# Kernel optimization log

Hardware: AMD Instinct MI355X
Metric: run time of the kernel (lower is better)

Reference implementation:

```python
import jax, jax.numpy as jnp
import numpy as np

P, G, UV = 5, 40000, 256          # n_parts, gs_num (visible UV texels), uv_size
ZD, FD, HD = 32, 64, 32           # latent_z_dim, latent_f_dim, latent_h_dim
H1, L1 = 128, 3                   # mlp1 hidden dim, fc layers
H2, L2 = 128, 3                   # mlp2 hidden dim, fc layers
CC, LC = 64, 4                    # cnn hidden channels, cnn hidden layers


def _mlp_params(key, din, hid, nlayers, dout, nparts):
    ks = jax.random.split(key, 3)
    s = lambda f: 1.0 / np.sqrt(f)
    return dict(
        w_in=jax.random.normal(ks[0], (nparts, din, hid), jnp.float32) * s(din),
        b_in=jnp.zeros((nparts, hid), jnp.float32),
        w_hid=jax.random.normal(ks[1], (nparts, nlayers - 1, hid, hid), jnp.float32) * s(hid),
        b_hid=jnp.zeros((nparts, nlayers - 1, hid), jnp.float32),
        w_out=jax.random.normal(ks[2], (nparts, hid, dout), jnp.float32) * s(hid),
        b_out=jnp.zeros((nparts, dout), jnp.float32),
    )


def setup_inputs() -> dict:
    key = jax.random.key(0)
    ks = jax.random.split(key, 12)
    d1 = FD + ZD
    d2 = d1 + 3 + 11
    inp = {
        'latent_z': jax.random.normal(ks[2], (G, ZD), jnp.float32),
        'latent_f': jax.random.normal(ks[3], (P, FD), jnp.float32),
        'cano_xyz': jax.random.normal(ks[4], (G, 3), jnp.float32),
    }
    for k, v in _mlp_params(ks[0], d1, H1, L1, 11, P).items():
        inp['mlp1_' + k] = v
    for k, v in _mlp_params(ks[1], d2, H2, L2, HD, P).items():
        inp['mlp2_' + k] = v
    inp['conv_in_w'] = jax.random.normal(ks[5], (CC, HD, 3, 3), jnp.float32) * (1.0 / np.sqrt(HD * 9))
    inp['conv_in_b'] = jnp.zeros((CC,), jnp.float32)
    inp['conv_hid_w'] = jax.random.normal(ks[6], (LC - 1, CC, CC, 3, 3), jnp.float32) * (1.0 / np.sqrt(CC * 9))
    inp['conv_hid_b'] = jnp.zeros((LC - 1, CC), jnp.float32)
    inp['conv_out_w'] = jax.random.normal(ks[7], (3, CC, 3, 3), jnp.float32) * (1.0 / np.sqrt(CC * 9))
    inp['conv_out_b'] = jnp.zeros((3,), jnp.float32)
    inp['gs_part'] = jax.random.randint(ks[8], (G,), 0, P, jnp.int32)
    inp['uv_idx'] = jax.random.permutation(ks[9], UV * UV)[:G].astype(jnp.int32)  # unique visible texels
    return inp


def _part_mlp(x, w_in, b_in, w_hid, b_hid, w_out, b_out, part):
    # x: [G, D]; weights stacked over parts. Run every part's MLP, gather by part id.
    h = jax.nn.leaky_relu(jnp.einsum('gd,pdh->pgh', x, w_in) + b_in[:, None, :])
    for l in range(w_hid.shape[1]):
        h = jax.nn.leaky_relu(jnp.einsum('pgh,pho->pgo', h, w_hid[:, l]) + b_hid[:, l][:, None, :])
    out = jnp.einsum('pgh,pho->pgo', h, w_out) + b_out[:, None, :]  # [P, G, O]
    return out[part, jnp.arange(out.shape[1])]                       # [G, O]


def _conv(x, w, b):
    y = jax.lax.conv_general_dilated(x, w, (1, 1), 'SAME',
                                     dimension_numbers=('NCHW', 'OIHW', 'NCHW'))
    return y + b[None, :, None, None]


def _instance_norm(x, eps=1e-5):
    m = x.mean(axis=(2, 3), keepdims=True)
    v = x.var(axis=(2, 3), keepdims=True)
    return (x - m) / jnp.sqrt(v + eps)


def reference(latent_z, latent_f, cano_xyz,
              mlp1_w_in, mlp1_b_in, mlp1_w_hid, mlp1_b_hid, mlp1_w_out, mlp1_b_out,
              mlp2_w_in, mlp2_b_in, mlp2_w_hid, mlp2_b_hid, mlp2_w_out, mlp2_b_out,
              conv_in_w, conv_in_b, conv_hid_w, conv_hid_b, conv_out_w, conv_out_b,
              gs_part, uv_idx):
    feat_f = latent_f[gs_part]                                  # [G, FD] per-part feature gather
    x1 = jnp.concatenate([feat_f, latent_z], axis=-1)           # [G, FD+ZD]
    attrs = _part_mlp(x1, mlp1_w_in, mlp1_b_in, mlp1_w_hid, mlp1_b_hid,
                      mlp1_w_out, mlp1_b_out, gs_part)          # [G, 11] gaussian attrs
    x2 = jnp.concatenate([x1, cano_xyz, attrs], axis=-1)        # [G, FD+ZD+3+11]
    h = _part_mlp(x2, mlp2_w_in, mlp2_b_in, mlp2_w_hid, mlp2_b_hid,
                  mlp2_w_out, mlp2_b_out, gs_part)              # [G, HD]
    # scatter per-gaussian features back into the UV map (uvmask-indexed texels)
    uvmap = jnp.zeros((UV * UV, h.shape[-1]), h.dtype).at[uv_idx].add(h)
    x = uvmap.T.reshape(1, h.shape[-1], UV, UV)                 # [1, HD, UV, UV]
    # CNN refinement: conv -> (relu, conv, instance_norm) x (LC-1) -> conv -> sigmoid
    x = _conv(x, conv_in_w, conv_in_b)
    for l in range(conv_hid_w.shape[0]):
        x = _instance_norm(_conv(jax.nn.relu(x), conv_hid_w[l], conv_hid_b[l]))
    x = _conv(x, conv_out_w, conv_out_b)
    return jax.nn.sigmoid(x)                                    # [1, 3, UV, UV]
```

## Files before the change

### kernel.cpp

```cpp
#include <hip/hip_runtime.h>

#define G_N 40000
#define P_N 5
#define PIX 65536
#define XP 136
#define SP 40

typedef short short8 __attribute__((ext_vector_type(8)));
typedef short short4v __attribute__((ext_vector_type(4)));
typedef float f32x4 __attribute__((ext_vector_type(4)));
#define MFMA16(a, b, c) __builtin_amdgcn_mfma_f32_16x16x32_bf16(a, b, c, 0, 0, 0)

__device__ __forceinline__ short f2b(float f) {
    unsigned u = __builtin_bit_cast(unsigned, f);
    unsigned r = (u + 0x7fffu + ((u >> 16) & 1u)) >> 16;
    return (short)r;
}
__device__ __forceinline__ float b2f(short s) {
    unsigned u = ((unsigned)(unsigned short)s) << 16;
    return __builtin_bit_cast(float, u);
}


__global__ __launch_bounds__(256) void hist_k(const int* __restrict__ part,
                                              int* __restrict__ counts, int n) {
    __shared__ int s_c[P_N];
    if (threadIdx.x < P_N) s_c[threadIdx.x] = 0;
    __syncthreads();
    int g = blockIdx.x * 256 + threadIdx.x;
    if (g < n) atomicAdd(&s_c[part[g]], 1);
    __syncthreads();
    if (threadIdx.x < P_N) atomicAdd(&counts[threadIdx.x], s_c[threadIdx.x]);
}

__global__ void offs_k(const int* __restrict__ counts, int* __restrict__ offs) {
    if (threadIdx.x == 0) {
        int o = 0;
        for (int p = 0; p < P_N; ++p) {
            offs[p] = o;
            o += (counts[p] + 63) & ~63;
        }
        offs[P_N] = o;
    }
}

__global__ __launch_bounds__(256) void scatter_k(const int* __restrict__ part,
                                                 const int* __restrict__ offs,
                                                 int* __restrict__ cursors,
                                                 int* __restrict__ perm, int n) {
    const int t = threadIdx.x;
    const int g = blockIdx.x * 256 + t;
    const int p = (g < n) ? part[g] : -1;
    const int lane = t & 63;
    const int wid = t >> 6;
    __shared__ int s_wc[4][P_N];
    __shared__ int s_base[P_N];
    const unsigned long long lmask = (1ull << lane) - 1ull;
    int myrank = 0;
    for (int pp = 0; pp < P_N; ++pp) {
        unsigned long long m = __ballot(p == pp);
        if (p == pp) myrank = __popcll(m & lmask);
        if (lane == 0) s_wc[wid][pp] = __popcll(m);
    }
    __syncthreads();
    if (t < P_N) {
        int tot = s_wc[0][t] + s_wc[1][t] + s_wc[2][t] + s_wc[3][t];
        s_base[t] = atomicAdd(&cursors[t], tot);
    }
    __syncthreads();
    if (g < n) {
        int pre = 0;
        #pragma unroll
        for (int w2 = 0; w2 < 4; ++w2) if (w2 < wid) pre += s_wc[w2][p];
        perm[offs[p] + s_base[p] + pre + myrank] = g;
    }
}


__device__ __forceinline__ float mseg(int l, const float* __restrict__ src,
                                      int DIN, int DOUT, int NP, int pps) {
    const int pn = NP * 128;
    const int p = l / pn;
    const int r = l - p * pn;
    const int n = r >> 7, k = r & 127;
    return (n < DOUT && k < DIN) ? src[p * pps + k * DOUT + n] : 0.f;
}
__device__ __forceinline__ float cseg(int l, const float* __restrict__ src, int CIN) {
    const int per = 9 * 64 * CIN;
    const int ll = l / per;
    int rem = l - ll * per;
    const int tap = rem / (64 * CIN);
    rem -= tap * 64 * CIN;
    const int och = rem / CIN;
    const int ci = rem - och * CIN;
    return src[((ll * 64 + och) * CIN + ci) * 9 + tap];
}

__global__ __launch_bounds__(256) void prep_k(
        const float* __restrict__ m1wi, const float* __restrict__ m1wh,
        const float* __restrict__ m1wo, const float* __restrict__ m2wi,
        const float* __restrict__ m2wh, const float* __restrict__ m2wo,
        const float* __restrict__ cinw, const float* __restrict__ chw,
        short* __restrict__ wb) {
    const int idx = blockIdx.x * 256 + threadIdx.x;
    if (idx >= 651264) return;
    float v;
    if      (idx < 81920)  v = mseg(idx,          m1wi,         96, 128, 128, 12288);
    else if (idx < 163840) v = mseg(idx - 81920,  m1wh,        128, 128, 128, 32768);
    else if (idx < 245760) v = mseg(idx - 163840, m1wh + 16384,128, 128, 128, 32768);
    else if (idx < 256000) v = mseg(idx - 245760, m1wo,        128,  11,  16, 1408);
    else if (idx < 337920) v = mseg(idx - 256000, m2wi,        110, 128, 128, 14080);
    else if (idx < 419840) v = mseg(idx - 337920, m2wh,        128, 128, 128, 32768);
    else if (idx < 501760) v = mseg(idx - 419840, m2wh + 16384,128, 128, 128, 32768);
    else if (idx < 522240) v = mseg(idx - 501760, m2wo,        128,  32,  32, 4096);
    else if (idx < 540672) v = cseg(idx - 522240, cinw, 32);
    else                   v = cseg(idx - 540672, chw, 64);
    wb[idx] = f2b(v);
}


template<int NKC, bool ACT>
__device__ __forceinline__ void wcompute(const short8 (&A)[4][NKC],
                                         const short* __restrict__ wt,
                                         const float* __restrict__ bias,
                                         short* dst) {
    const int ln = threadIdx.x & 15, lq = threadIdx.x >> 4;
    short8 Bc[2][NKC];
    float bsc[2];
    #pragma unroll
    for (int j = 0; j < 2; ++j) {
        #pragma unroll
        for (int kc = 0; kc < NKC; ++kc)
            Bc[j][kc] = *(const short8*)(wt + (j * 16 + ln) * 128 + kc * 32 + lq * 8);
        bsc[j] = bias[j * 16 + ln];
    }
    #pragma unroll
    for (int g = 0; g < 4; ++g) {
        short8 Bn[2][NKC];
        float bsn[2];
        if (g < 3) {
            #pragma unroll
            for (int j = 0; j < 2; ++j) {
                #pragma unroll
                for (int kc = 0; kc < NKC; ++kc)
                    Bn[j][kc] = *(const short8*)(wt + ((g * 2 + 2 + j) * 16 + ln) * 128 + kc * 32 + lq * 8);
                bsn[j] = bias[(g * 2 + 2 + j) * 16 + ln];
            }
        }
        f32x4 acc[4][2];
        #pragma unroll
        for (int mt = 0; mt < 4; ++mt)
            #pragma unroll
            for (int j = 0; j < 2; ++j) {
                f32x4 a = {bsc[j], bsc[j], bsc[j], bsc[j]};
                acc[mt][j] = a;
            }
        #pragma unroll
        for (int kc = 0; kc < NKC; ++kc)
            #pragma unroll
            for (int mt = 0; mt < 4; ++mt)
                #pragma unroll
                for (int j = 0; j < 2; ++j)
                    acc[mt][j] = MFMA16(A[mt][kc], Bc[j][kc], acc[mt][j]);
        #pragma unroll
        for (int mt = 0; mt < 4; ++mt)
            #pragma unroll
            for (int j = 0; j < 2; ++j)
                #pragma unroll
                for (int r = 0; r < 4; ++r) {
                    float v = acc[mt][j][r];
                    if (ACT) v = fmaxf(v, 0.01f * v);
                    dst[(mt * 16 + lq * 4 + r) * XP + (g * 2 + j) * 16 + ln] = f2b(v);
                }
        if (g < 3) {
            #pragma unroll
            for (int j = 0; j < 2; ++j) {
                #pragma unroll
                for (int kc = 0; kc < NKC; ++kc) Bc[j][kc] = Bn[j][kc];
                bsc[j] = bsn[j];
            }
        }
    }
}

__device__ __forceinline__ void preload4(short8 (&A)[4][4], const short* s) {
    const int ln = threadIdx.x & 15, lq = threadIdx.x >> 4;
    #pragma unroll
    for (int mt = 0; mt < 4; ++mt)
        #pragma unroll
        for (int kc = 0; kc < 4; ++kc)
            A[mt][kc] = *(const short8*)(s + (mt * 16 + ln) * XP + kc * 32 + lq * 8);
}

__global__ __launch_bounds__(64, 2) void mlp_k(
        const float* __restrict__ latent_z, const float* __restrict__ latent_f,
        const float* __restrict__ cano,
        const short* __restrict__ wt1i, const float* __restrict__ b1i,
        const short* __restrict__ wt1h0, const short* __restrict__ wt1h1,
        const float* __restrict__ b1h,
        const short* __restrict__ wt1o, const float* __restrict__ b1o,
        const short* __restrict__ wt2i, const float* __restrict__ b2i,
        const short* __restrict__ wt2h0, const short* __restrict__ wt2h1,
        const float* __restrict__ b2h,
        const short* __restrict__ wt2o, const float* __restrict__ b2o,
        const int* __restrict__ uv_idx, const int* __restrict__ perm,
        const int* __restrict__ offs, const int* __restrict__ counts,
        unsigned short* __restrict__ uvmap ) {
    __shared__ short s_h[64 * XP];
    __shared__ short s_c4[64 * SP];
    __shared__ int s_g[64];
    __shared__ int s_uv[64];

    const int t = threadIdx.x;
    const int ln = t & 15, lq = t >> 4;
    const int pos0 = blockIdx.x * 64;
    if (pos0 >= offs[P_N]) return;
    int p = 0;
    #pragma unroll
    for (int q = 1; q < P_N; ++q) if (pos0 >= offs[q]) p = q;
    const int vend = offs[p] + counts[p];

    {
        const int pos = pos0 + t;
        const int g = (pos < vend) ? perm[pos] : -1;
        s_g[t] = g;
        s_uv[t] = (g >= 0) ? uv_idx[g] : 0;
    }
    for (int i = t; i < 64 * SP / 2; i += 64) ((int*)s_c4)[i] = 0;
    __syncthreads();

    for (int i = t; i < 64 * 16; i += 64) {
        const int g = i >> 4, k4 = (i & 15) * 4;
        const float4 v = *(const float4*)(latent_f + p * 64 + k4);
        short4v o = {f2b(v.x), f2b(v.y), f2b(v.z), f2b(v.w)};
        *(short4v*)(s_h + g * XP + k4) = o;
    }
    for (int i = t; i < 64 * 8; i += 64) {
        const int g = i >> 3, k4 = (i & 7) * 4;
        const int gg = s_g[g];
        short4v o = {0, 0, 0, 0};
        if (gg >= 0) {
            const float4 v = *(const float4*)(latent_z + gg * 32 + k4);
            o[0] = f2b(v.x); o[1] = f2b(v.y); o[2] = f2b(v.z); o[3] = f2b(v.w);
        }
        *(short4v*)(s_h + g * XP + 64 + k4) = o;
    }
    for (int i = t; i < 64 * 3; i += 64) {
        const int g = i / 3, k = i - g * 3;
        const int gg = s_g[g];
        s_c4[g * SP + k] = (gg >= 0) ? f2b(cano[gg * 3 + k]) : 0;
    }
    __syncthreads();

    short8 A1[4][3];
    #pragma unroll
    for (int mt = 0; mt < 4; ++mt)
        #pragma unroll
        for (int kc = 0; kc < 3; ++kc)
            A1[mt][kc] = *(const short8*)(s_h + (mt * 16 + ln) * XP + kc * 32 + lq * 8);
    __syncthreads();

    wcompute<3, true>(A1, wt1i + p * 16384, b1i + p * 128, s_h);
    __syncthreads();
    {
        short8 Ah[4][4];
        preload4(Ah, s_h); __syncthreads();
        wcompute<4, true>(Ah, wt1h0 + p * 16384, b1h + (p * 2 + 0) * 128, s_h);
        __syncthreads();
        preload4(Ah, s_h); __syncthreads();
        wcompute<4, true>(Ah, wt1h1 + p * 16384, b1h + (p * 2 + 1) * 128, s_h);
        __syncthreads();
        preload4(Ah, s_h); __syncthreads();
        short8 B[4];
        #pragma unroll
        for (int kc = 0; kc < 4; ++kc)
            B[kc] = *(const short8*)(wt1o + p * 2048 + ln * 128 + kc * 32 + lq * 8);
        const float bs = (ln < 11) ? b1o[p * 11 + ln] : 0.f;
        #pragma unroll
        for (int mt = 0; mt < 4; ++mt) {
            f32x4 acc = {bs, bs, bs, bs};
            #pragma unroll
            for (int kc = 0; kc < 4; ++kc) acc = MFMA16(Ah[mt][kc], B[kc], acc);
            if (ln < 11) {
                #pragma unroll
                for (int r = 0; r < 4; ++r)
                    s_c4[(mt * 16 + lq * 4 + r) * SP + 3 + ln] = f2b(acc[r]);
            }
        }
    }
    __syncthreads();

    {
        short8 A2[4][4];
        #pragma unroll
        for (int mt = 0; mt < 4; ++mt) {
            A2[mt][0] = A1[mt][0]; A2[mt][1] = A1[mt][1]; A2[mt][2] = A1[mt][2];
            A2[mt][3] = *(const short8*)(s_c4 + (mt * 16 + ln) * SP + lq * 8);
        }
        __syncthreads();
        wcompute<4, true>(A2, wt2i + p * 16384, b2i + p * 128, s_h);
    }
    __syncthreads();
    {
        short8 Ah[4][4];
        preload4(Ah, s_h); __syncthreads();
        wcompute<4, true>(Ah, wt2h0 + p * 16384, b2h + (p * 2 + 0) * 128, s_h);
        __syncthreads();
        preload4(Ah, s_h); __syncthreads();
        wcompute<4, true>(Ah, wt2h1 + p * 16384, b2h + (p * 2 + 1) * 128, s_h);
        __syncthreads();
        preload4(Ah, s_h);
        #pragma unroll
        for (int nt = 0; nt < 2; ++nt) {
            short8 B[4];
            #pragma unroll
            for (int kc = 0; kc < 4; ++kc)
                B[kc] = *(const short8*)(wt2o + p * 4096 + (nt * 16 + ln) * 128 + kc * 32 + lq * 8);
            const float bs = b2o[p * 32 + nt * 16 + ln];
            #pragma unroll
            for (int mt = 0; mt < 4; ++mt) {
                f32x4 acc = {bs, bs, bs, bs};
                #pragma unroll
                for (int kc = 0; kc < 4; ++kc) acc = MFMA16(Ah[mt][kc], B[kc], acc);
                #pragma unroll
                for (int r = 0; r < 4; ++r) {
                    const int m = mt * 16 + lq * 4 + r;
                    const int g = s_g[m];
                    if (g >= 0)
                        uvmap[s_uv[m] * 32 + nt * 16 + ln] = (unsigned short)f2b(acc[r]);
                }
            }
        }
    }
}


template<int CIN, int TRANS, bool STATS>
__global__ __launch_bounds__(128, 2) void conv_k(
        const unsigned short* __restrict__ in,
        const short* __restrict__ wt,
        const float* __restrict__ bias,
        const float* __restrict__ psum, const float* __restrict__ psq,
        unsigned short* __restrict__ out,
        float* __restrict__ ssum, float* __restrict__ ssq) {
    constexpr int CS = CIN + 8;
    constexpr int NKC = CIN / 32;
    constexpr int RUNS = CIN / 8;
    __shared__ short s_in[10 * 18 * CS];
    __shared__ float s_mr[2][64];
    __shared__ float s_red[2][2][64];

    const int t = threadIdx.x;
    const int ln = t & 15, lq = (t >> 4) & 3;
    const int w2 = t >> 6;
    const int tx0 = blockIdx.x * 16, ty0 = blockIdx.y * 8;

    if (TRANS == 2 && t < 64) {
        const float m = psum[t] * (1.f / PIX);
        const float vv = psq[t] * (1.f / PIX) - m * m;
        s_mr[0][t] = m;
        s_mr[1][t] = rsqrtf(vv + 1e-5f);
    }
    if (TRANS == 2) __syncthreads();

    short8 Bc[NKC][4];
    #pragma unroll
    for (int kc = 0; kc < NKC; ++kc)
        #pragma unroll
        for (int nt = 0; nt < 4; ++nt)
            Bc[kc][nt] = *(const short8*)(wt + (nt * 16 + ln) * CIN + kc * 32 + lq * 8);

    for (int i = t; i < 180 * RUNS; i += 128) {
        const int sp = i / RUNS, run = i - sp * RUNS;
        const int r = sp / 18, c = sp - r * 18;
        const int gy = ty0 + r - 1, gx = tx0 + c - 1;
        short* dst = &s_in[(r * 18 + c) * CS + run * 8];
        if (gy >= 0 && gy < 256 && gx >= 0 && gx < 256) {
            short8 v = *(const short8*)(in + ((gy * 256 + gx) * CIN + run * 8));
            if (TRANS == 0) {
                *(short8*)dst = v;
            } else {
                short8 o;
                #pragma unroll
                for (int j = 0; j < 8; ++j) {
                    float f = b2f(v[j]);
                    if (TRANS == 2) f = (f - s_mr[0][run * 8 + j]) * s_mr[1][run * 8 + j];
                    o[j] = f2b(fmaxf(f, 0.f));
                }
                *(short8*)dst = o;
            }
        } else {
            short8 z = {0, 0, 0, 0, 0, 0, 0, 0};
            *(short8*)dst = z;
        }
    }
    __syncthreads();

    f32x4 acc[4][4];
    {
        float bs[4];
        #pragma unroll
        for (int nt = 0; nt < 4; ++nt) bs[nt] = bias[nt * 16 + ln];
        #pragma unroll
        for (int mt = 0; mt < 4; ++mt)
            #pragma unroll
            for (int nt = 0; nt < 4; ++nt) {
                f32x4 a = {bs[nt], bs[nt], bs[nt], bs[nt]};
                acc[mt][nt] = a;
            }
    }

    #pragma unroll
    for (int tap = 0; tap < 9; ++tap) {
        short8 Bn[NKC][4];
        if (tap < 8) {
            const short* wnext = wt + (tap + 1) * 64 * CIN;
            #pragma unroll
            for (int kc = 0; kc < NKC; ++kc)
                #pragma unroll
                for (int nt = 0; nt < 4; ++nt)
                    Bn[kc][nt] = *(const short8*)(wnext + (nt * 16 + ln) * CIN + kc * 32 + lq * 8);
        }
        const int dy = tap / 3, dx = tap - dy * 3;
        #pragma unroll
        for (int kc = 0; kc < NKC; ++kc) {
            short8 A[4];
            #pragma unroll
            for (int mt = 0; mt < 4; ++mt)
                A[mt] = *(const short8*)&s_in[((w2 * 4 + mt + dy) * 18 + ln + dx) * CS + kc * 32 + lq * 8];
            #pragma unroll
            for (int mt = 0; mt < 4; ++mt)
                #pragma unroll
                for (int nt = 0; nt < 4; ++nt)
                    acc[mt][nt] = MFMA16(A[mt], Bc[kc][nt], acc[mt][nt]);
        }
        if (tap < 8) {
            #pragma unroll
            for (int kc = 0; kc < NKC; ++kc)
                #pragma unroll
                for (int nt = 0; nt < 4; ++nt)
                    Bc[kc][nt] = Bn[kc][nt];
        }
    }

    #pragma unroll
    for (int nt = 0; nt < 4; ++nt) {
        float ls = 0.f, lsq = 0.f;
        #pragma unroll
        for (int mt = 0; mt < 4; ++mt) {
            const int gy = ty0 + w2 * 4 + mt;
            #pragma unroll
            for (int r = 0; r < 4; ++r) {
                const float v = acc[mt][nt][r];
                const int gx = tx0 + lq * 4 + r;
                out[(gy * 256 + gx) * 64 + nt * 16 + ln] = (unsigned short)f2b(v);
                if (STATS) { ls += v; lsq = fmaf(v, v, lsq); }
            }
        }
        if (STATS) {
            ls  += __shfl_xor(ls, 16, 64);
            ls  += __shfl_xor(ls, 32, 64);
            lsq += __shfl_xor(lsq, 16, 64);
            lsq += __shfl_xor(lsq, 32, 64);
            if (lq == 0 && (t & 32) == 0) {
                s_red[w2][0][nt * 16 + ln] = ls;
                s_red[w2][1][nt * 16 + ln] = lsq;
            }
        }
    }
    if (STATS) {
        __syncthreads();
        if (t < 64) {
            atomicAdd(&ssum[t], s_red[0][0][t] + s_red[1][0][t]);
            atomicAdd(&ssq[t],  s_red[0][1][t] + s_red[1][1][t]);
        }
    }
}

__global__ __launch_bounds__(128) void convout_k(
        const unsigned short* __restrict__ in,
        const float* __restrict__ w,
        const float* __restrict__ bias,
        const float* __restrict__ psum, const float* __restrict__ psq,
        float* __restrict__ out) {
    constexpr int CS = 72;
    __shared__ short s_in[10 * 18 * CS];
    __shared__ float s_w[3][9][64];
    __shared__ float s_mr[2][64];

    const int t = threadIdx.x;
    const int tx0 = blockIdx.x * 16, ty0 = blockIdx.y * 8;
    if (t < 64) {
        const float m = psum[t] * (1.f / PIX);
        const float vv = psq[t] * (1.f / PIX) - m * m;
        s_mr[0][t] = m;
        s_mr[1][t] = rsqrtf(vv + 1e-5f);
    }
    __syncthreads();

    for (int i = t; i < 180 * 8; i += 128) {
        const int sp = i >> 3, run = i & 7;
        const int r = sp / 18, c = sp - r * 18;
        const int gy = ty0 + r - 1, gx = tx0 + c - 1;
        short* dst = &s_in[(r * 18 + c) * CS + run * 8];
        if (gy >= 0 && gy < 256 && gx >= 0 && gx < 256) {
            short8 v = *(const short8*)(in + ((gy * 256 + gx) * 64 + run * 8));
            short8 o;
            #pragma unroll
            for (int j = 0; j < 8; ++j) {
                const float f = (b2f(v[j]) - s_mr[0][run * 8 + j]) * s_mr[1][run * 8 + j];
                o[j] = f2b(f);
            }
            *(short8*)dst = o;
        } else {
            short8 z = {0, 0, 0, 0, 0, 0, 0, 0};
            *(short8*)dst = z;
        }
    }
    for (int i = t; i < 1728; i += 128) {
        const int o = i / 576;
        const int rem = i - o * 576;
        const int tap = rem >> 6;
        const int ci = rem & 63;
        s_w[o][tap][ci] = w[o * 576 + ci * 9 + tap];
    }
    __syncthreads();

    const int py = t >> 4, px = t & 15;
    float a0 = bias[0], a1 = bias[1], a2 = bias[2];
    for (int tap = 0; tap < 9; ++tap) {
        const int dy = tap / 3, dx = tap % 3;
        const short* rp = &s_in[((py + dy) * 18 + (px + dx)) * CS];
        #pragma unroll
        for (int c8 = 0; c8 < 8; ++c8) {
            short8 v = *(const short8*)(rp + c8 * 8);
            #pragma unroll
            for (int j = 0; j < 8; ++j) {
                const float f = b2f(v[j]);
                const int ci = c8 * 8 + j;
                a0 = fmaf(f, s_w[0][tap][ci], a0);
                a1 = fmaf(f, s_w[1][tap][ci], a1);
                a2 = fmaf(f, s_w[2][tap][ci], a2);
            }
        }
    }
    const int pix = (ty0 + py) * 256 + tx0 + px;
    out[pix]           = 1.f / (1.f + expf(-a0));
    out[PIX + pix]     = 1.f / (1.f + expf(-a1));
    out[2 * PIX + pix] = 1.f / (1.f + expf(-a2));
}


extern "C" void kernel_launch(void* const* d_in, const int* in_sizes, int n_in,
                              void* d_out, int out_size, void* d_ws, size_t ws_size,
                              hipStream_t stream) {
    (void)in_sizes; (void)n_in; (void)out_size; (void)ws_size;
    const float* latent_z = (const float*)d_in[0];
    const float* latent_f = (const float*)d_in[1];
    const float* cano     = (const float*)d_in[2];
    const float* m1wi = (const float*)d_in[3];
    const float* m1bi = (const float*)d_in[4];
    const float* m1wh = (const float*)d_in[5];
    const float* m1bh = (const float*)d_in[6];
    const float* m1wo = (const float*)d_in[7];
    const float* m1bo = (const float*)d_in[8];
    const float* m2wi = (const float*)d_in[9];
    const float* m2bi = (const float*)d_in[10];
    const float* m2wh = (const float*)d_in[11];
    const float* m2bh = (const float*)d_in[12];
    const float* m2wo = (const float*)d_in[13];
    const float* m2bo = (const float*)d_in[14];
    const float* cinw = (const float*)d_in[15];
    const float* cinb = (const float*)d_in[16];
    const float* chw  = (const float*)d_in[17];
    const float* chb  = (const float*)d_in[18];
    const float* cow  = (const float*)d_in[19];
    const float* cob  = (const float*)d_in[20];
    const int* gs_part = (const int*)d_in[21];
    const int* uv_idx  = (const int*)d_in[22];

    float* ws = (float*)d_ws;
    unsigned short* actA = (unsigned short*)ws;
    unsigned short* actB = (unsigned short*)(ws + 2097152);
    unsigned short* uvmap = actB;

    short* wb = (short*)(ws + 4194304);
    short* wt1i  = wb;
    short* wt1h0 = wb + 81920;
    short* wt1h1 = wb + 163840;
    short* wt1o  = wb + 245760;
    short* wt2i  = wb + 256000;
    short* wt2h0 = wb + 337920;
    short* wt2h1 = wb + 419840;
    short* wt2o  = wb + 501760;
    short* cwt_in  = wb + 522240;
    short* cwt_hid = wb + 540672;

    float* small = ws + 4194304 + 330000;
    int* counts  = (int*)small;
    int* cursors = counts + 8;
    int* offs    = cursors + 8;
    float* ssum  = small + 32;
    float* ssq   = ssum + 192;
    int* perm    = (int*)(ssq + 192);

    hipMemsetAsync(uvmap, 0, (size_t)PIX * 32 * sizeof(unsigned short), stream);
    hipMemsetAsync(small, 0, 1024 * sizeof(float), stream);

    hist_k<<<157, 256, 0, stream>>>(gs_part, counts, G_N);
    offs_k<<<1, 64, 0, stream>>>(counts, offs);
    scatter_k<<<157, 256, 0, stream>>>(gs_part, offs, cursors, perm, G_N);

    prep_k<<<2544, 256, 0, stream>>>(m1wi, m1wh, m1wo, m2wi, m2wh, m2wo, cinw, chw, wb);

    mlp_k<<<630, 64, 0, stream>>>(latent_z, latent_f, cano,
        wt1i, m1bi, wt1h0, wt1h1, m1bh, wt1o, m1bo,
        wt2i, m2bi, wt2h0, wt2h1, m2bh, wt2o, m2bo,
        uv_idx, perm, offs, counts, uvmap);

    dim3 cgrid(16, 32);
    conv_k<32, 0, false><<<cgrid, 128, 0, stream>>>(uvmap, cwt_in, cinb,
        nullptr, nullptr, actA, nullptr, nullptr);
    conv_k<64, 1, true><<<cgrid, 128, 0, stream>>>(actA, cwt_hid, chb,
        nullptr, nullptr, actB, ssum, ssq);
    conv_k<64, 2, true><<<cgrid, 128, 0, stream>>>(actB, cwt_hid + 36864, chb + 64,
        ssum, ssq, actA, ssum + 64, ssq + 64);
    conv_k<64, 2, true><<<cgrid, 128, 0, stream>>>(actA, cwt_hid + 73728, chb + 128,
        ssum + 64, ssq + 64, actB, ssum + 128, ssq + 128);
    convout_k<<<cgrid, 128, 0, stream>>>(actB, cow, cob,
        ssum + 128, ssq + 128, (float*)d_out);
}
```

Measured before the change: 269.1 us.

## Split MLP layers across two waves with ping-pong LDS and transposed MFMA

The MLP kernel now runs 128 threads per block, with each wave computing half of the output columns of every layer. Activations ping-pong between two LDS buffers, which removes the extra barrier the old in-place update needed between reading and writing. The MFMA operands are swapped so each lane holds four consecutive output channels, allowing vectorized bf16 stores to LDS, to the uvmap and in the conv kernels. Conv statistics are now reduced with shuffles and atomics directly instead of through a shared buffer. The costs are more LDS per block, duplicated A-operand loads in both waves, and more global atomics.

```diff
diff --git a/kernel.cpp b/kernel.cpp
--- a/kernel.cpp
+++ b/kernel.cpp
@@ -4,7 +4,7 @@
 #define P_N 5
 #define PIX 65536
 #define XP 136
-#define SP 40
+#define SP 32
 
 typedef short short8 __attribute__((ext_vector_type(8)));
 typedef short short4v __attribute__((ext_vector_type(4)));
@@ -120,71 +120,51 @@
 
 
 template<int NKC, bool ACT>
-__device__ __forceinline__ void wcompute(const short8 (&A)[4][NKC],
-                                         const short* __restrict__ wt,
-                                         const float* __restrict__ bias,
-                                         short* dst) {
-    const int ln = threadIdx.x & 15, lq = threadIdx.x >> 4;
-    short8 Bc[2][NKC];
-    float bsc[2];
+__device__ __forceinline__ void wlayer(const short8 (&A)[4][NKC],
+                                       const short* __restrict__ wt,
+                                       const float* __restrict__ bias,
+                                       short* dst, int ln, int lq, int w) {
     #pragma unroll
-    for (int j = 0; j < 2; ++j) {
+    for (int g = 0; g < 2; ++g) {
+        short8 W[2][NKC];
+        f32x4 b4[2];
+        #pragma unroll
+        for (int j = 0; j < 2; ++j) {
+            const int ntg = w * 4 + g * 2 + j;
+            #pragma unroll
+            for (int kc = 0; kc < NKC; ++kc)
+                W[j][kc] = *(const short8*)(wt + (ntg * 16 + ln) * 128 + kc * 32 + lq * 8);
+            b4[j] = *(const f32x4*)(bias + ntg * 16 + lq * 4);
+        }
+        f32x4 acc[4][2];
+        #pragma unroll
+        for (int mt = 0; mt < 4; ++mt)
+            #pragma unroll
+            for (int j = 0; j < 2; ++j) acc[mt][j] = b4[j];
         #pragma unroll
         for (int kc = 0; kc < NKC; ++kc)
-            Bc[j][kc] = *(const short8*)(wt + (j * 16 + ln) * 128 + kc * 32 + lq * 8);
-        bsc[j] = bias[j * 16 + ln];
-    }
-    #pragma unroll
-    for (int g = 0; g < 4; ++g) {
-        short8 Bn[2][NKC];
-        float bsn[2];
-        if (g < 3) {
+            #pragma unroll
+            for (int mt = 0; mt < 4; ++mt)
+                #pragma unroll
+                for (int j = 0; j < 2; ++j)
+                    acc[mt][j] = MFMA16(W[j][kc], A[mt][kc], acc[mt][j]);
+        #pragma unroll
+        for (int mt = 0; mt < 4; ++mt)
             #pragma unroll
             for (int j = 0; j < 2; ++j) {
-                #pragma unroll
-                for (int kc = 0; kc < NKC; ++kc)
-                    Bn[j][kc] = *(const short8*)(wt + ((g * 2 + 2 + j) * 16 + ln) * 128 + kc * 32 + lq * 8);
-                bsn[j] = bias[(g * 2 + 2 + j) * 16 + ln];
+                const int ntg = w * 4 + g * 2 + j;
+                f32x4 a = acc[mt][j];
+                if (ACT) {
+                    #pragma unroll
+                    for (int r = 0; r < 4; ++r) a[r] = fmaxf(a[r], 0.01f * a[r]);
+                }
+                short4v o = {f2b(a[0]), f2b(a[1]), f2b(a[2]), f2b(a[3])};
+                *(short4v*)(dst + (mt * 16 + ln) * XP + ntg * 16 + lq * 4) = o;
             }
-        }
-        f32x4 acc[4][2];
-        #pragma unroll
-        for (int mt = 0; mt < 4; ++mt)
-            #pragma unroll
-            for (int j = 0; j < 2; ++j) {
-                f32x4 a = {bsc[j], bsc[j], bsc[j], bsc[j]};
-                acc[mt][j] = a;
-            }
-        #pragma unroll
-        for (int kc = 0; kc < NKC; ++kc)
-            #pragma unroll
-            for (int mt = 0; mt < 4; ++mt)
-                #pragma unroll
-                for (int j = 0; j < 2; ++j)
-                    acc[mt][j] = MFMA16(A[mt][kc], Bc[j][kc], acc[mt][j]);
-        #pragma unroll
-        for (int mt = 0; mt < 4; ++mt)
-            #pragma unroll
-            for (int j = 0; j < 2; ++j)
-                #pragma unroll
-                for (int r = 0; r < 4; ++r) {
-                    float v = acc[mt][j][r];
-                    if (ACT) v = fmaxf(v, 0.01f * v);
-                    dst[(mt * 16 + lq * 4 + r) * XP + (g * 2 + j) * 16 + ln] = f2b(v);
-                }
-        if (g < 3) {
-            #pragma unroll
-            for (int j = 0; j < 2; ++j) {
-                #pragma unroll
-                for (int kc = 0; kc < NKC; ++kc) Bc[j][kc] = Bn[j][kc];
-                bsc[j] = bsn[j];
-            }
-        }
-    }
-}
-
-__device__ __forceinline__ void preload4(short8 (&A)[4][4], const short* s) {
-    const int ln = threadIdx.x & 15, lq = threadIdx.x >> 4;
+    }
+}
+
+__device__ __forceinline__ void preload4(short8 (&A)[4][4], const short* s, int ln, int lq) {
     #pragma unroll
     for (int mt = 0; mt < 4; ++mt)
         #pragma unroll
@@ -192,7 +172,7 @@
             A[mt][kc] = *(const short8*)(s + (mt * 16 + ln) * XP + kc * 32 + lq * 8);
 }
 
-__global__ __launch_bounds__(64, 2) void mlp_k(
+__global__ __launch_bounds__(128, 2) void mlp_k(
         const float* __restrict__ latent_z, const float* __restrict__ latent_f,
         const float* __restrict__ cano,
         const short* __restrict__ wt1i, const float* __restrict__ b1i,
@@ -206,13 +186,15 @@
         const int* __restrict__ uv_idx, const int* __restrict__ perm,
         const int* __restrict__ offs, const int* __restrict__ counts,
         unsigned short* __restrict__ uvmap ) {
-    __shared__ short s_h[64 * XP];
+    __shared__ short s_a[64 * XP];
+    __shared__ short s_b[64 * XP];
     __shared__ short s_c4[64 * SP];
     __shared__ int s_g[64];
     __shared__ int s_uv[64];
 
     const int t = threadIdx.x;
-    const int ln = t & 15, lq = t >> 4;
+    const int ln = t & 15, lq = (t >> 4) & 3;
+    const int w = t >> 6;
     const int pos0 = blockIdx.x * 64;
     if (pos0 >= offs[P_N]) return;
     int p = 0;
@@ -220,22 +202,22 @@
     for (int q = 1; q < P_N; ++q) if (pos0 >= offs[q]) p = q;
     const int vend = offs[p] + counts[p];
 
-    {
+    if (t < 64) {
         const int pos = pos0 + t;
         const int g = (pos < vend) ? perm[pos] : -1;
         s_g[t] = g;
         s_uv[t] = (g >= 0) ? uv_idx[g] : 0;
     }
-    for (int i = t; i < 64 * SP / 2; i += 64) ((int*)s_c4)[i] = 0;
-    __syncthreads();
-
-    for (int i = t; i < 64 * 16; i += 64) {
+    for (int i = t; i < 64 * SP / 2; i += 128) ((int*)s_c4)[i] = 0;
+    __syncthreads();
+
+    for (int i = t; i < 64 * 16; i += 128) {
         const int g = i >> 4, k4 = (i & 15) * 4;
         const float4 v = *(const float4*)(latent_f + p * 64 + k4);
         short4v o = {f2b(v.x), f2b(v.y), f2b(v.z), f2b(v.w)};
-        *(short4v*)(s_h + g * XP + k4) = o;
-    }
-    for (int i = t; i < 64 * 8; i += 64) {
+        *(short4v*)(s_a + g * XP + k4) = o;
+    }
+    for (int i = t; i < 64 * 8; i += 128) {
         const int g = i >> 3, k4 = (i & 7) * 4;
         const int gg = s_g[g];
         short4v o = {0, 0, 0, 0};
@@ -243,9 +225,9 @@
             const float4 v = *(const float4*)(latent_z + gg * 32 + k4);
             o[0] = f2b(v.x); o[1] = f2b(v.y); o[2] = f2b(v.z); o[3] = f2b(v.w);
         }
-        *(short4v*)(s_h + g * XP + 64 + k4) = o;
-    }
-    for (int i = t; i < 64 * 3; i += 64) {
+        *(short4v*)(s_a + g * XP + 64 + k4) = o;
+    }
+    for (int i = t; i < 64 * 3; i += 128) {
         const int g = i / 3, k = i - g * 3;
         const int gg = s_g[g];
         s_c4[g * SP + k] = (gg >= 0) ? f2b(cano[gg * 3 + k]) : 0;
@@ -257,35 +239,41 @@
     for (int mt = 0; mt < 4; ++mt)
         #pragma unroll
         for (int kc = 0; kc < 3; ++kc)
-            A1[mt][kc] = *(const short8*)(s_h + (mt * 16 + ln) * XP + kc * 32 + lq * 8);
-    __syncthreads();
-
-    wcompute<3, true>(A1, wt1i + p * 16384, b1i + p * 128, s_h);
+            A1[mt][kc] = *(const short8*)(s_a + (mt * 16 + ln) * XP + kc * 32 + lq * 8);
+
+    wlayer<3, true>(A1, wt1i + p * 16384, b1i + p * 128, s_b, ln, lq, w);
     __syncthreads();
     {
         short8 Ah[4][4];
-        preload4(Ah, s_h); __syncthreads();
-        wcompute<4, true>(Ah, wt1h0 + p * 16384, b1h + (p * 2 + 0) * 128, s_h);
+        preload4(Ah, s_b, ln, lq);
+        wlayer<4, true>(Ah, wt1h0 + p * 16384, b1h + (p * 2 + 0) * 128, s_a, ln, lq, w);
         __syncthreads();
-        preload4(Ah, s_h); __syncthreads();
-        wcompute<4, true>(Ah, wt1h1 + p * 16384, b1h + (p * 2 + 1) * 128, s_h);
+        preload4(Ah, s_a, ln, lq);
+        wlayer<4, true>(Ah, wt1h1 + p * 16384, b1h + (p * 2 + 1) * 128, s_b, ln, lq, w);
         __syncthreads();
-        preload4(Ah, s_h); __syncthreads();
-        short8 B[4];
+    }
+    {
+        short8 W[4];
         #pragma unroll
         for (int kc = 0; kc < 4; ++kc)
-            B[kc] = *(const short8*)(wt1o + p * 2048 + ln * 128 + kc * 32 + lq * 8);
-        const float bs = (ln < 11) ? b1o[p * 11 + ln] : 0.f;
-        #pragma unroll
-        for (int mt = 0; mt < 4; ++mt) {
-            f32x4 acc = {bs, bs, bs, bs};
-            #pragma unroll
-            for (int kc = 0; kc < 4; ++kc) acc = MFMA16(Ah[mt][kc], B[kc], acc);
-            if (ln < 11) {
-                #pragma unroll
-                for (int r = 0; r < 4; ++r)
-                    s_c4[(mt * 16 + lq * 4 + r) * SP + 3 + ln] = f2b(acc[r]);
-            }
+            W[kc] = *(const short8*)(wt1o + p * 2048 + ln * 128 + kc * 32 + lq * 8);
+        float b4[4];
+        #pragma unroll
+        for (int r = 0; r < 4; ++r)
+            b4[r] = (lq * 4 + r < 11) ? b1o[p * 11 + lq * 4 + r] : 0.f;
+        #pragma unroll
+        for (int mt2 = 0; mt2 < 2; ++mt2) {
+            const int mt = w * 2 + mt2;
+            short8 Am[4];
+            #pragma unroll
+            for (int kc = 0; kc < 4; ++kc)
+                Am[kc] = *(const short8*)(s_b + (mt * 16 + ln) * XP + kc * 32 + lq * 8);
+            f32x4 acc = {b4[0], b4[1], b4[2], b4[3]};
+            #pragma unroll
+            for (int kc = 0; kc < 4; ++kc) acc = MFMA16(W[kc], Am[kc], acc);
+            #pragma unroll
+            for (int r = 0; r < 4; ++r)
+                s_c4[(mt * 16 + ln) * SP + 3 + lq * 4 + r] = f2b(acc[r]);
         }
     }
     __syncthreads();
@@ -297,38 +285,37 @@
             A2[mt][0] = A1[mt][0]; A2[mt][1] = A1[mt][1]; A2[mt][2] = A1[mt][2];
             A2[mt][3] = *(const short8*)(s_c4 + (mt * 16 + ln) * SP + lq * 8);
         }
-        __syncthreads();
-        wcompute<4, true>(A2, wt2i + p * 16384, b2i + p * 128, s_h);
+        wlayer<4, true>(A2, wt2i + p * 16384, b2i + p * 128, s_a, ln, lq, w);
     }
     __syncthreads();
     {
         short8 Ah[4][4];
-        preload4(Ah, s_h); __syncthreads();
-        wcompute<4, true>(Ah, wt2h0 + p * 16384, b2h + (p * 2 + 0) * 128, s_h);
+        preload4(Ah, s_a, ln, lq);
+        wlayer<4, true>(Ah, wt2h0 + p * 16384, b2h + (p * 2 + 0) * 128, s_b, ln, lq, w);
         __syncthreads();
-        preload4(Ah, s_h); __syncthreads();
-        wcompute<4, true>(Ah, wt2h1 + p * 16384, b2h + (p * 2 + 1) * 128, s_h);
+        preload4(Ah, s_b, ln, lq);
+        wlayer<4, true>(Ah, wt2h1 + p * 16384, b2h + (p * 2 + 1) * 128, s_a, ln, lq, w);
         __syncthreads();
-        preload4(Ah, s_h);
-        #pragma unroll
-        for (int nt = 0; nt < 2; ++nt) {
-            short8 B[4];
+    }
+    {
+        short8 W[4];
+        #pragma unroll
+        for (int kc = 0; kc < 4; ++kc)
+            W[kc] = *(const short8*)(wt2o + p * 4096 + (w * 16 + ln) * 128 + kc * 32 + lq * 8);
+        const f32x4 b4 = *(const f32x4*)(b2o + p * 32 + w * 16 + lq * 4);
+        #pragma unroll
+        for (int mt = 0; mt < 4; ++mt) {
+            short8 Am[4];
             #pragma unroll
             for (int kc = 0; kc < 4; ++kc)
-                B[kc] = *(const short8*)(wt2o + p * 4096 + (nt * 16 + ln) * 128 + kc * 32 + lq * 8);
-            const float bs = b2o[p * 32 + nt * 16 + ln];
-            #pragma unroll
-            for (int mt = 0; mt < 4; ++mt) {
-                f32x4 acc = {bs, bs, bs, bs};
-                #pragma unroll
-                for (int kc = 0; kc < 4; ++kc) acc = MFMA16(Ah[mt][kc], B[kc], acc);
-                #pragma unroll
-                for (int r = 0; r < 4; ++r) {
-                    const int m = mt * 16 + lq * 4 + r;
-                    const int g = s_g[m];
-                    if (g >= 0)
-                        uvmap[s_uv[m] * 32 + nt * 16 + ln] = (unsigned short)f2b(acc[r]);
-                }
+                Am[kc] = *(const short8*)(s_a + (mt * 16 + ln) * XP + kc * 32 + lq * 8);
+            f32x4 acc = b4;
+            #pragma unroll
+            for (int kc = 0; kc < 4; ++kc) acc = MFMA16(W[kc], Am[kc], acc);
+            const int m = mt * 16 + ln;
+            if (s_g[m] >= 0) {
+                short4v o = {f2b(acc[0]), f2b(acc[1]), f2b(acc[2]), f2b(acc[3])};
+                *(short4v*)((short*)uvmap + s_uv[m] * 32 + w * 16 + lq * 4) = o;
             }
         }
     }
@@ -348,7 +335,6 @@
     constexpr int RUNS = CIN / 8;
     __shared__ short s_in[10 * 18 * CS];
     __shared__ float s_mr[2][64];
-    __shared__ float s_red[2][2][64];
 
     const int t = threadIdx.x;
     const int ln = t & 15, lq = (t >> 4) & 3;
@@ -398,16 +384,12 @@
 
     f32x4 acc[4][4];
     {
-        float bs[4];
-        #pragma unroll
-        for (int nt = 0; nt < 4; ++nt) bs[nt] = bias[nt * 16 + ln];
-        #pragma unroll
-        for (int mt = 0; mt < 4; ++mt)
-            #pragma unroll
-            for (int nt = 0; nt < 4; ++nt) {
-                f32x4 a = {bs[nt], bs[nt], bs[nt], bs[nt]};
-                acc[mt][nt] = a;
-            }
+        #pragma unroll
+        for (int nt = 0; nt < 4; ++nt) {
+            const f32x4 b4 = *(const f32x4*)(bias + nt * 16 + lq * 4);
+            #pragma unroll
+            for (int mt = 0; mt < 4; ++mt) acc[mt][nt] = b4;
+        }
     }
 
     #pragma unroll
@@ -432,7 +414,7 @@
             for (int mt = 0; mt < 4; ++mt)
                 #pragma unroll
                 for (int nt = 0; nt < 4; ++nt)
-                    acc[mt][nt] = MFMA16(A[mt], Bc[kc][nt], acc[mt][nt]);
+                    acc[mt][nt] = MFMA16(Bc[kc][nt], A[mt], acc[mt][nt]);
         }
         if (tap < 8) {
             #pragma unroll
@@ -445,34 +427,38 @@
 
     #pragma unroll
     for (int nt = 0; nt < 4; ++nt) {
-        float ls = 0.f, lsq = 0.f;
         #pragma unroll
         for (int mt = 0; mt < 4; ++mt) {
             const int gy = ty0 + w2 * 4 + mt;
-            #pragma unroll
-            for (int r = 0; r < 4; ++r) {
-                const float v = acc[mt][nt][r];
-                const int gx = tx0 + lq * 4 + r;
-                out[(gy * 256 + gx) * 64 + nt * 16 + ln] = (unsigned short)f2b(v);
-                if (STATS) { ls += v; lsq = fmaf(v, v, lsq); }
+            const f32x4 a = acc[mt][nt];
+            short4v o = {f2b(a[0]), f2b(a[1]), f2b(a[2]), f2b(a[3])};
+            *(short4v*)((short*)out + ((gy * 256 + tx0 + ln) * 64 + nt * 16 + lq * 4)) = o;
+        }
+        if (STATS) {
+            f32x4 s4 = {0.f, 0.f, 0.f, 0.f}, q4 = {0.f, 0.f, 0.f, 0.f};
+            #pragma unroll
+            for (int mt = 0; mt < 4; ++mt) {
+                const f32x4 a = acc[mt][nt];
+                #pragma unroll
+                for (int r = 0; r < 4; ++r) {
+                    s4[r] += a[r];
+                    q4[r] = fmaf(a[r], a[r], q4[r]);
+                }
             }
-        }
-        if (STATS) {
-            ls  += __shfl_xor(ls, 16, 64);
-            ls  += __shfl_xor(ls, 32, 64);
-            lsq += __shfl_xor(lsq, 16, 64);
-            lsq += __shfl_xor(lsq, 32, 64);
-            if (lq == 0 && (t & 32) == 0) {
-                s_red[w2][0][nt * 16 + ln] = ls;
-                s_red[w2][1][nt * 16 + ln] = lsq;
+            #pragma unroll
+            for (int m = 1; m <= 8; m <<= 1)
+                #pragma unroll
+                for (int r = 0; r < 4; ++r) {
+                    s4[r] += __shfl_xor(s4[r], m, 64);
+                    q4[r] += __shfl_xor(q4[r], m, 64);
+                }
+            if (ln == 0) {
+                #pragma unroll
+                for (int r = 0; r < 4; ++r) {
+                    atomicAdd(&ssum[nt * 16 + lq * 4 + r], s4[r]);
+                    atomicAdd(&ssq[nt * 16 + lq * 4 + r], q4[r]);
+                }
             }
-        }
-    }
-    if (STATS) {
-        __syncthreads();
-        if (t < 64) {
-            atomicAdd(&ssum[t], s_red[0][0][t] + s_red[1][0][t]);
-            atomicAdd(&ssq[t],  s_red[0][1][t] + s_red[1][1][t]);
         }
     }
 }
@@ -613,7 +599,7 @@
 
     prep_k<<<2544, 256, 0, stream>>>(m1wi, m1wh, m1wo, m2wi, m2wh, m2wo, cinw, chw, wb);
 
-    mlp_k<<<630, 64, 0, stream>>>(latent_z, latent_f, cano,
+    mlp_k<<<630, 128, 0, stream>>>(latent_z, latent_f, cano,
         wt1i, m1bi, wt1h0, wt1h1, m1bh, wt1o, m1bo,
         wt2i, m2bi, wt2h0, wt2h1, m2bh, wt2o, m2bo,
         uv_idx, perm, offs, counts, uvmap);
```

Measured after the change: 467.7 us. 73.8% more time.
